# Performance work log

Hardware: AMD Instinct MI355X
Metric: run time of the kernel (lower is better)

## Reference

```python
import jax, jax.numpy as jnp
import numpy as np

B, R, C, E = 4, 32, 512, 512
H = 8
D = E // H  # 64
EPS = 1e-6


def setup_inputs() -> dict:
    key = jax.random.key(0)
    ks = jax.random.split(key, 9)
    s = 1.0 / np.sqrt(E)  # keep activations in a sane range
    return {
        "x": jax.random.normal(ks[0], (B, R, C, E), jnp.float32),
        "Wq": jax.random.normal(ks[1], (E, E), jnp.float32) * s,
        "bq": jax.random.normal(ks[2], (E,), jnp.float32) * 0.01,
        "Wk": jax.random.normal(ks[3], (E, E), jnp.float32) * s,
        "bk": jax.random.normal(ks[4], (E,), jnp.float32) * 0.01,
        "Wv": jax.random.normal(ks[5], (E, E), jnp.float32) * s,
        "bv": jax.random.normal(ks[6], (E,), jnp.float32) * 0.01,
        "Wo": jax.random.normal(ks[7], (E, E), jnp.float32) * s,
        "bo": jax.random.normal(ks[8], (E,), jnp.float32) * 0.01,
    }


def reference(x, Wq, bq, Wk, bk, Wv, bv, Wo, bo):
    b, r, c, e = x.shape
    # projections (torch Linear: y = x @ W.T + b), split heads -> [b,r,c,H,D]
    q = (x @ Wq.T + bq).reshape(b, r, c, H, D)
    k = (x @ Wk.T + bk).reshape(b, r, c, H, D)
    v = (x @ Wv.T + bv).reshape(b, r, c, H, D)
    # ELU+1 feature map (Performer/linear attention)
    q = jax.nn.elu(q) + 1.0
    k = jax.nn.elu(k) + 1.0
    # K^T V accumulation over the column axis: [b,r,H,D,D]
    ktv = jnp.einsum('brchd,brche->brhde', k, v)
    # normalizer: q . sum_c(k)  -> [b,r,c,H]
    ksum = k.sum(axis=2)  # [b,r,H,D]
    z = 1.0 / (jnp.einsum('brchd,brhd->brch', q, ksum) + EPS)
    # O(N) attention output: [b,r,c,H,D]
    out_h = jnp.einsum('brchd,brhde->brche', q, ktv) * z[..., None]
    out = out_h.reshape(b, r, c, e)
    return out @ Wo.T + bo
```

## Files before the change

### kernel.cpp

```cpp
#include <hip/hip_runtime.h>

typedef unsigned short u16;
typedef short short8 __attribute__((ext_vector_type(8)));
typedef float f32x4 __attribute__((ext_vector_type(4)));

__device__ __forceinline__ u16 f2b(float f) {
  unsigned u = __float_as_uint(f);
  u = u + 0x7FFFu + ((u >> 16) & 1u);
  return (u16)(u >> 16);
}
__device__ __forceinline__ float b2f(u16 b) {
  return __uint_as_float(((unsigned)b) << 16);
}

#define ASYNC_LD16(g, l)                                                                   \
  __builtin_amdgcn_global_load_lds((const __attribute__((address_space(1))) void*)(g),     \
                                   (__attribute__((address_space(3))) void*)(l), 16, 0, 0)

#define BAR()                                  \
  do {                                         \
    asm volatile("" ::: "memory");             \
    __builtin_amdgcn_s_barrier();              \
    asm volatile("" ::: "memory");             \
  } while (0)

__global__ void convert_x(const float* __restrict__ x, u16* __restrict__ xb) {
  size_t i = ((size_t)blockIdx.x * 256 + threadIdx.x) * 4;
  float4 f = *(const float4*)(x + i);
  ushort4 o;
  o.x = f2b(f.x); o.y = f2b(f.y); o.z = f2b(f.z); o.w = f2b(f.w);
  *(ushort4*)(xb + i) = o;
}

__global__ void convert_w(const float* __restrict__ Wq, const float* __restrict__ Wk,
                          const float* __restrict__ Wv, const float* __restrict__ Wo,
                          u16* __restrict__ Wqkv, u16* __restrict__ Wob) {
  int idx = (blockIdx.x * 256 + threadIdx.x) * 4;
  int row = idx >> 9;
  int col = idx & 511;
  const float* src = (row < 512)    ? Wq + (size_t)row * 512
                     : (row < 1024) ? Wk + (size_t)(row - 512) * 512
                     : (row < 1536) ? Wv + (size_t)(row - 1024) * 512
                                    : Wo + (size_t)(row - 1536) * 512;
  u16* dst = (row < 1536) ? Wqkv + (size_t)row * 512 : Wob + (size_t)(row - 1536) * 512;
  float4 f = *(const float4*)(src + col);
  ushort4 o;
  o.x = f2b(f.x); o.y = f2b(f.y); o.z = f2b(f.z); o.w = f2b(f.w);
  *(ushort4*)(dst + col) = o;
}


#define STAGE_A(buf, kt)                                                 \
  do {                                                                   \
    ASYNC_LD16(Asrc0 + (kt) * 32, S + (buf) * 16384 + tid * 8);          \
    ASYNC_LD16(Asrc1 + (kt) * 32, S + (buf) * 16384 + 4096 + tid * 8);   \
  } while (0)
#define STAGE_B(buf, kt)                                                 \
  do {                                                                   \
    ASYNC_LD16(Bsrc0 + (kt) * 32, S + (buf) * 16384 + 8192 + tid * 8);   \
    ASYNC_LD16(Bsrc1 + (kt) * 32, S + (buf) * 16384 + 12288 + tid * 8);  \
  } while (0)

#define GEMM_MAIN_LOOP()                                                                     \
  STAGE_A(0, 0); STAGE_B(0, 0);                                                              \
  STAGE_A(1, 1); STAGE_B(1, 1);                                                              \
  STAGE_A(2, 2); STAGE_B(2, 2);                                                              \
  asm volatile("s_waitcnt vmcnt(8)" ::: "memory");               \
  BAR();                                                                                     \
  for (int t = 0; t < 16; ++t) {                                                             \
    const u16* Ab = S + (t & 3) * 16384;                                                     \
    const int nb = (t + 3) & 3;                                                              \
    short8 bf[4], af[4];                                                                     \
                     \
    if (t < 13) STAGE_A(nb, t + 3);                                                          \
    _Pragma("unroll") for (int j = 0; j < 4; ++j) bf[j] = *(const short8*)&Ab[rbB + j * 512];\
    _Pragma("unroll") for (int m = 0; m < 4; ++m) af[m] = *(const short8*)&Ab[rbA + m * 512];\
    BAR();                                                                                   \
    __builtin_amdgcn_s_setprio(1);                                                           \
    _Pragma("unroll") for (int m = 0; m < 4; ++m)                                            \
      _Pragma("unroll") for (int j = 0; j < 4; ++j)                                          \
        acc[m][j] = __builtin_amdgcn_mfma_f32_16x16x32_bf16(af[m], bf[j], acc[m][j], 0, 0, 0);\
    __builtin_amdgcn_s_setprio(0);                                                           \
                               \
    if (t < 13) STAGE_B(nb, t + 3);                                                          \
    _Pragma("unroll") for (int m = 0; m < 4; ++m)                                            \
        af[m] = *(const short8*)&Ab[rbA + (m + 4) * 512];                                    \
    BAR();                                                                                   \
    __builtin_amdgcn_s_setprio(1);                                                           \
    _Pragma("unroll") for (int m = 0; m < 4; ++m)                                            \
      _Pragma("unroll") for (int j = 0; j < 4; ++j)                                          \
        acc[m + 4][j] =                                                                      \
            __builtin_amdgcn_mfma_f32_16x16x32_bf16(af[m], bf[j], acc[m + 4][j], 0, 0, 0);   \
    __builtin_amdgcn_s_setprio(0);                                                           \
         \
    if (t < 13)      asm volatile("s_waitcnt vmcnt(8)" ::: "memory");                        \
    else if (t == 13) asm volatile("s_waitcnt vmcnt(4)" ::: "memory");                       \
    else             asm volatile("s_waitcnt vmcnt(0)" ::: "memory");                        \
    BAR();                                                                                   \
  }

__global__ __launch_bounds__(512, 2) void gemm_qkv(
    const u16* __restrict__ xb, const u16* __restrict__ Wqkv,
    const float* __restrict__ bq, const float* __restrict__ bk,
    const float* __restrict__ bv, u16* __restrict__ Qb,
    u16* __restrict__ Ktg, u16* __restrict__ Vtg) {
  __shared__ u16 S[65536];
  const int tid = threadIdx.x;
  const int bid = blockIdx.x;
  const int wg = (bid & 7) * 192 + (bid >> 3);
  const int mtile = wg / 6;
  const int ntile = wg - mtile * 6;
  const int blockM = mtile << 8;
  const int blockN = ntile << 8;

  const int lane = tid & 63;
  const int w = tid >> 6;
  const int wm = (w >> 2) << 7;
  const int wn = (w & 3) << 6;
  const int lr = lane & 15;
  const int qd = lane >> 4;

  const int srow = tid >> 2;
  const int sg = (tid & 3) ^ ((tid >> 3) & 3);
  const u16* Asrc0 = xb + (size_t)(blockM + srow) * 512 + sg * 8;
  const u16* Asrc1 = Asrc0 + 128 * 512;
  const u16* Bsrc0 = Wqkv + (size_t)(blockN + srow) * 512 + sg * 8;
  const u16* Bsrc1 = Bsrc0 + 128 * 512;

  const int gsw = (qd ^ ((lr >> 1) & 3)) * 8;
  const int rbA = (wm + lr) * 32 + gsw;
  const int rbB = 8192 + (wn + lr) * 32 + gsw;

  f32x4 acc[8][4];
#pragma unroll
  for (int m = 0; m < 8; ++m)
#pragma unroll
    for (int j = 0; j < 4; ++j) acc[m][j] = {0.f, 0.f, 0.f, 0.f};

  GEMM_MAIN_LOOP();

  const int which = blockN >> 9;
  const int cb = blockN & 511;
  if (which == 0) {
#pragma unroll
    for (int j = 0; j < 4; ++j) {
      int col = cb + wn + j * 16 + lr;
      float bsv = bq[col];
#pragma unroll
      for (int m = 0; m < 8; ++m) {
        int row = blockM + wm + m * 16 + qd * 4;
#pragma unroll
        for (int r = 0; r < 4; ++r) {
          float v = acc[m][j][r] + bsv;
          v = (v > 0.f) ? v + 1.f : __expf(v);
          Qb[(size_t)(row + r) * 512 + col] = f2b(v);
        }
      }
    }
  } else {
    u16* dstT = (which == 1) ? Ktg : Vtg;
    const float* bias = (which == 1) ? bk : bv;
    const int br = blockM >> 9;
    const int t0 = (blockM & 511) + wm;
#pragma unroll
    for (int j = 0; j < 4; ++j) {
      int col = cb + wn + j * 16 + lr;
      float bsv = bias[col];
      size_t rowbase = (size_t)br * 262144 + (size_t)col * 512;
#pragma unroll
      for (int m = 0; m < 8; ++m) {
        int c0 = t0 + m * 16 + qd * 4;
        float v0 = acc[m][j][0] + bsv, v1 = acc[m][j][1] + bsv;
        float v2 = acc[m][j][2] + bsv, v3 = acc[m][j][3] + bsv;
        if (which == 1) {
          v0 = (v0 > 0.f) ? v0 + 1.f : __expf(v0);
          v1 = (v1 > 0.f) ? v1 + 1.f : __expf(v1);
          v2 = (v2 > 0.f) ? v2 + 1.f : __expf(v2);
          v3 = (v3 > 0.f) ? v3 + 1.f : __expf(v3);
        }
        ushort4 p;
        p.x = f2b(v0); p.y = f2b(v1); p.z = f2b(v2); p.w = f2b(v3);
        *(ushort4*)&dstT[rowbase + c0] = p;
      }
    }
  }
}

__global__ void attn(const u16* __restrict__ Qb, const u16* __restrict__ Ktg,
                     const u16* __restrict__ Vtg, u16* __restrict__ Hb) {
  __shared__ u16 KtS[64 * 32];
  __shared__ u16 VtS[64 * 32];
  __shared__ u16 QS[2 * 128 * 32];
  __shared__ u16 ktvT[2 * 64 * 32];
  __shared__ float part[256];
  __shared__ float ksumf[64];
  __shared__ float zs[128];

  const int tid = threadIdx.x;
  const int br = blockIdx.x >> 3;
  const int h = blockIdx.x & 7;
  const int h64 = h * 64;
  const size_t tok0 = (size_t)br * 512;
  const size_t tbase = (size_t)br * 262144 + (size_t)h64 * 512;

  const int lane = tid & 63;
  const int w = tid >> 6;
  const int lr = lane & 15;
  const int qd = lane >> 4;

  const int sc_chan = tid >> 2, sc_seg = tid & 3;

  f32x4 acc[4];
#pragma unroll
  for (int j = 0; j < 4; ++j) acc[j] = {0.f, 0.f, 0.f, 0.f};
  float ks = 0.f;

  for (int ct = 0; ct < 16; ++ct) {
    __syncthreads();
    {
      size_t g = tbase + (size_t)sc_chan * 512 + ct * 32 + sc_seg * 8;
      ASYNC_LD16(Ktg + g, KtS + tid * 8);
      ASYNC_LD16(Vtg + g, VtS + tid * 8);
    }
    __syncthreads();
    short8 a = *(const short8*)&KtS[(w * 16 + lr) * 32 + qd * 8];
#pragma unroll
    for (int j = 0; j < 4; ++j) {
      short8 b = *(const short8*)&VtS[(j * 16 + lr) * 32 + qd * 8];
      acc[j] = __builtin_amdgcn_mfma_f32_16x16x32_bf16(a, b, acc[j], 0, 0, 0);
    }
    ushort4 k0 = *(const ushort4*)&KtS[sc_chan * 32 + sc_seg * 8];
    ushort4 k1 = *(const ushort4*)&KtS[sc_chan * 32 + sc_seg * 8 + 4];
    ks += b2f(k0.x) + b2f(k0.y) + b2f(k0.z) + b2f(k0.w)
        + b2f(k1.x) + b2f(k1.y) + b2f(k1.z) + b2f(k1.w);
  }
  part[tid] = ks;
  {
    int kc = w >> 1;
    int dp = (w & 1) * 16 + qd * 4;
#pragma unroll
    for (int j = 0; j < 4; ++j) {
      int e = j * 16 + lr;
      ushort4 p;
      p.x = f2b(acc[j][0]); p.y = f2b(acc[j][1]);
      p.z = f2b(acc[j][2]); p.w = f2b(acc[j][3]);
      *(ushort4*)&ktvT[kc * 2048 + e * 32 + dp] = p;
    }
  }
  __syncthreads();
  if (tid < 64)
    ksumf[tid] = part[tid * 4] + part[tid * 4 + 1] + part[tid * 4 + 2] + part[tid * 4 + 3];
  __syncthreads();

  short8 bfr[4][2];
#pragma unroll
  for (int j = 0; j < 4; ++j)
#pragma unroll
    for (int kc = 0; kc < 2; ++kc)
      bfr[j][kc] = *(const short8*)&ktvT[kc * 2048 + (j * 16 + lr) * 32 + qd * 8];

  for (int ct = 0; ct < 4; ++ct) {
    __syncthreads();
#pragma unroll
    for (int kc = 0; kc < 2; ++kc)
#pragma unroll
      for (int half = 0; half < 2; ++half)
        ASYNC_LD16(Qb + (tok0 + ct * 128 + half * 64 + sc_chan) * 512 + h64 + kc * 32 + sc_seg * 8,
                   QS + kc * 4096 + half * 2048 + tid * 8);
    __syncthreads();
    if (tid < 128) {
      float s = 0.f;
#pragma unroll 8
      for (int i = 0; i < 32; ++i) {
        int ix = (i + tid) & 31;
        s += b2f(QS[tid * 32 + ix]) * ksumf[ix];
        s += b2f(QS[4096 + tid * 32 + ix]) * ksumf[32 + ix];
      }
      zs[tid] = 1.f / (s + 1e-6f);
    }
    __syncthreads();
#pragma unroll
    for (int s = 0; s < 2; ++s) {
      int mrow = (w * 2 + s) * 16 + lr;
      short8 a0 = *(const short8*)&QS[mrow * 32 + qd * 8];
      short8 a1 = *(const short8*)&QS[4096 + mrow * 32 + qd * 8];
      f32x4 o[4];
#pragma unroll
      for (int j = 0; j < 4; ++j) {
        o[j] = {0.f, 0.f, 0.f, 0.f};
        o[j] = __builtin_amdgcn_mfma_f32_16x16x32_bf16(a0, bfr[j][0], o[j], 0, 0, 0);
        o[j] = __builtin_amdgcn_mfma_f32_16x16x32_bf16(a1, bfr[j][1], o[j], 0, 0, 0);
      }
      int tl = (w * 2 + s) * 16 + qd * 4;
      float z0 = zs[tl], z1 = zs[tl + 1], z2 = zs[tl + 2], z3 = zs[tl + 3];
      size_t gb = (tok0 + ct * 128 + tl) * 512 + h64;
#pragma unroll
      for (int j = 0; j < 4; ++j) {
        int e = j * 16 + lr;
        Hb[gb + e] = f2b(o[j][0] * z0);
        Hb[gb + 512 + e] = f2b(o[j][1] * z1);
        Hb[gb + 1024 + e] = f2b(o[j][2] * z2);
        Hb[gb + 1536 + e] = f2b(o[j][3] * z3);
      }
    }
  }
}

__global__ __launch_bounds__(512, 2) void gemm_out(
    const u16* __restrict__ Hb, const u16* __restrict__ Wob,
    const float* __restrict__ bo, float* __restrict__ out) {
  __shared__ u16 S[65536];
  const int tid = threadIdx.x;
  const int bid = blockIdx.x;
  const int wg = (bid & 7) * 64 + (bid >> 3);
  const int mtile = wg >> 1;
  const int ntile = wg & 1;
  const int blockM = mtile << 8;
  const int blockN = ntile << 8;

  const int lane = tid & 63;
  const int w = tid >> 6;
  const int wm = (w >> 2) << 7;
  const int wn = (w & 3) << 6;
  const int lr = lane & 15;
  const int qd = lane >> 4;

  const int srow = tid >> 2;
  const int sg = (tid & 3) ^ ((tid >> 3) & 3);
  const u16* Asrc0 = Hb + (size_t)(blockM + srow) * 512 + sg * 8;
  const u16* Asrc1 = Asrc0 + 128 * 512;
  const u16* Bsrc0 = Wob + (size_t)(blockN + srow) * 512 + sg * 8;
  const u16* Bsrc1 = Bsrc0 + 128 * 512;

  const int gsw = (qd ^ ((lr >> 1) & 3)) * 8;
  const int rbA = (wm + lr) * 32 + gsw;
  const int rbB = 8192 + (wn + lr) * 32 + gsw;

  f32x4 acc[8][4];
#pragma unroll
  for (int m = 0; m < 8; ++m)
#pragma unroll
    for (int j = 0; j < 4; ++j) acc[m][j] = {0.f, 0.f, 0.f, 0.f};

  GEMM_MAIN_LOOP();

#pragma unroll
  for (int j = 0; j < 4; ++j) {
    int col = blockN + wn + j * 16 + lr;
    float bsv = bo[col];
#pragma unroll
    for (int m = 0; m < 8; ++m) {
      int row = blockM + wm + m * 16 + qd * 4;
#pragma unroll
      for (int r = 0; r < 4; ++r)
        out[(size_t)(row + r) * 512 + col] = acc[m][j][r] + bsv;
    }
  }
}

extern "C" void kernel_launch(void* const* d_in, const int* in_sizes, int n_in,
                              void* d_out, int out_size, void* d_ws, size_t ws_size,
                              hipStream_t stream) {
  const float* x  = (const float*)d_in[0];
  const float* Wq = (const float*)d_in[1];
  const float* bq = (const float*)d_in[2];
  const float* Wk = (const float*)d_in[3];
  const float* bk = (const float*)d_in[4];
  const float* Wv = (const float*)d_in[5];
  const float* bv = (const float*)d_in[6];
  const float* Wo = (const float*)d_in[7];
  const float* bo = (const float*)d_in[8];
  float* out = (float*)d_out;

  char* ws = (char*)d_ws;
  u16* xb   = (u16*)(ws);
  u16* Wqkv = (u16*)(ws + 0x04000000ull);
  u16* Wob  = (u16*)(ws + 0x04200000ull);
  u16* Qb   = (u16*)(ws + 0x04400000ull);
  u16* Ktg  = (u16*)(ws + 0x08400000ull);
  u16* Vtg  = (u16*)(ws + 0x0C400000ull);
  u16* Hb   = xb;

  hipLaunchKernelGGL(convert_x, dim3(32768), dim3(256), 0, stream, x, xb);
  hipLaunchKernelGGL(convert_w, dim3(1024), dim3(256), 0, stream, Wq, Wk, Wv, Wo, Wqkv, Wob);
  hipLaunchKernelGGL(gemm_qkv, dim3(1536), dim3(512), 0, stream, xb, Wqkv, bq, bk, bv, Qb, Ktg, Vtg);
  hipLaunchKernelGGL(attn, dim3(1024), dim3(256), 0, stream, Qb, Ktg, Vtg, Hb);
  hipLaunchKernelGGL(gemm_out, dim3(512), dim3(512), 0, stream, Hb, Wob, bo, out);
}
```

Baseline: 487.0 us.

## Restructure GEMM main loop to K=64 double-buffered stages with quadrant MFMA clusters

Replaces the 4-stage K=32 async-load pipeline with a 2-buffer K=64 scheme, where each buffer holds A and B tiles with a new 8-way XOR swizzle. Each K-step is split into four MFMA clusters over output quadrants. The next tile's global-to-LDS loads are interleaved between clusters, with fewer loop iterations and a different barrier cadence. The goal is to cut barrier and loop overhead per MFMA and to overlap loads with compute better. In exchange the prefetch distance is shallower, there are more barriers per step, and the register pressure from the two-slice fragments is higher.

```diff
diff --git a/kernel.cpp b/kernel.cpp
--- a/kernel.cpp
+++ b/kernel.cpp
@@ -50,53 +50,86 @@
 }
 
 
-#define STAGE_A(buf, kt)                                                 \
-  do {                                                                   \
-    ASYNC_LD16(Asrc0 + (kt) * 32, S + (buf) * 16384 + tid * 8);          \
-    ASYNC_LD16(Asrc1 + (kt) * 32, S + (buf) * 16384 + 4096 + tid * 8);   \
+#define LDSV(off) (*(const short8*)&S[(off)])
+
+#define STG(gp, scol, dst)                              \
+  do {                                                  \
+    ASYNC_LD16((gp) + (scol), S + (dst));               \
+    ASYNC_LD16((gp) + (scol) + 4096, S + (dst) + 512);  \
   } while (0)
-#define STAGE_B(buf, kt)                                                 \
-  do {                                                                   \
-    ASYNC_LD16(Bsrc0 + (kt) * 32, S + (buf) * 16384 + 8192 + tid * 8);   \
-    ASYNC_LD16(Bsrc1 + (kt) * 32, S + (buf) * 16384 + 12288 + tid * 8);  \
+
+#define MFMA_CL(MB, JB)                                                                     \
+  do {                                                                                      \
+    __builtin_amdgcn_s_setprio(1);                                                          \
+    _Pragma("unroll") for (int m_ = 0; m_ < 4; ++m_)                                        \
+      _Pragma("unroll") for (int j_ = 0; j_ < 2; ++j_) {                                    \
+        acc[(MB) + m_][(JB) + j_] = __builtin_amdgcn_mfma_f32_16x16x32_bf16(                \
+            aq[m_][0], bf[(JB) + j_][0], acc[(MB) + m_][(JB) + j_], 0, 0, 0);               \
+        acc[(MB) + m_][(JB) + j_] = __builtin_amdgcn_mfma_f32_16x16x32_bf16(                \
+            aq[m_][1], bf[(JB) + j_][1], acc[(MB) + m_][(JB) + j_], 0, 0, 0);               \
+      }                                                                                     \
+    __builtin_amdgcn_s_setprio(0);                                                          \
   } while (0)
 
-#define GEMM_MAIN_LOOP()                                                                     \
-  STAGE_A(0, 0); STAGE_B(0, 0);                                                              \
-  STAGE_A(1, 1); STAGE_B(1, 1);                                                              \
-  STAGE_A(2, 2); STAGE_B(2, 2);                                                              \
-  asm volatile("s_waitcnt vmcnt(8)" ::: "memory");               \
+#define KSTEP(BUF, SG1, SG2, SG3, SG4, BND)                                                  \
+  do {                                                                                       \
+    short8 aq[4][2], bf[4][2];                                                               \
+                                                \
+    _Pragma("unroll") for (int m_ = 0; m_ < 4; ++m_) {                                       \
+      aq[m_][0] = LDSV((BUF) + rA0 + m_ * 1024);                                             \
+      aq[m_][1] = LDSV((BUF) + rA1 + m_ * 1024);                                             \
+    }                                                                                        \
+    _Pragma("unroll") for (int j_ = 0; j_ < 2; ++j_) {                                       \
+      bf[j_][0] = LDSV((BUF) + rB0 + j_ * 1024);                                             \
+      bf[j_][1] = LDSV((BUF) + rB1 + j_ * 1024);                                             \
+    }                                                                                        \
+    SG1;                                                                                     \
+    BAR(); MFMA_CL(0, 0); BAR();                                                             \
+                                                                    \
+    _Pragma("unroll") for (int j_ = 0; j_ < 2; ++j_) {                                       \
+      bf[2 + j_][0] = LDSV((BUF) + rB0 + (2 + j_) * 1024);                                   \
+      bf[2 + j_][1] = LDSV((BUF) + rB1 + (2 + j_) * 1024);                                   \
+    }                                                                                        \
+    SG2; BAR(); MFMA_CL(0, 2); BAR();                                                        \
+                                  \
+    _Pragma("unroll") for (int m_ = 0; m_ < 4; ++m_) {                                       \
+      aq[m_][0] = LDSV((BUF) + rA0 + (4 + m_) * 1024);                                       \
+      aq[m_][1] = LDSV((BUF) + rA1 + (4 + m_) * 1024);                                       \
+    }                                                                                        \
+    SG3; BAR(); MFMA_CL(4, 2); BAR();                                                        \
+                                                                           \
+    SG4; BAR(); MFMA_CL(4, 0); BND; BAR();                                                   \
+  } while (0)
+
+#define GEMM8_LOOP()                                                                         \
+  STG(gB0, 0, dB0); STG(gB1, 0, dB1);                                                        \
+  STG(gA0, 0, dA0); STG(gA1, 0, dA1);                                                        \
+  STG(gB0, 64, 32768 + dB0); STG(gB1, 64, 32768 + dB1);                                      \
+  asm volatile("s_waitcnt vmcnt(4)" ::: "memory");                                           \
   BAR();                                                                                     \
-  for (int t = 0; t < 16; ++t) {                                                             \
-    const u16* Ab = S + (t & 3) * 16384;                                                     \
-    const int nb = (t + 3) & 3;                                                              \
-    short8 bf[4], af[4];                                                                     \
-                     \
-    if (t < 13) STAGE_A(nb, t + 3);                                                          \
-    _Pragma("unroll") for (int j = 0; j < 4; ++j) bf[j] = *(const short8*)&Ab[rbB + j * 512];\
-    _Pragma("unroll") for (int m = 0; m < 4; ++m) af[m] = *(const short8*)&Ab[rbA + m * 512];\
-    BAR();                                                                                   \
-    __builtin_amdgcn_s_setprio(1);                                                           \
-    _Pragma("unroll") for (int m = 0; m < 4; ++m)                                            \
-      _Pragma("unroll") for (int j = 0; j < 4; ++j)                                          \
-        acc[m][j] = __builtin_amdgcn_mfma_f32_16x16x32_bf16(af[m], bf[j], acc[m][j], 0, 0, 0);\
-    __builtin_amdgcn_s_setprio(0);                                                           \
-                               \
-    if (t < 13) STAGE_B(nb, t + 3);                                                          \
-    _Pragma("unroll") for (int m = 0; m < 4; ++m)                                            \
-        af[m] = *(const short8*)&Ab[rbA + (m + 4) * 512];                                    \
-    BAR();                                                                                   \
-    __builtin_amdgcn_s_setprio(1);                                                           \
-    _Pragma("unroll") for (int m = 0; m < 4; ++m)                                            \
-      _Pragma("unroll") for (int j = 0; j < 4; ++j)                                          \
-        acc[m + 4][j] =                                                                      \
-            __builtin_amdgcn_mfma_f32_16x16x32_bf16(af[m], bf[j], acc[m + 4][j], 0, 0, 0);   \
-    __builtin_amdgcn_s_setprio(0);                                                           \
-         \
-    if (t < 13)      asm volatile("s_waitcnt vmcnt(8)" ::: "memory");                        \
-    else if (t == 13) asm volatile("s_waitcnt vmcnt(4)" ::: "memory");                       \
-    else             asm volatile("s_waitcnt vmcnt(0)" ::: "memory");                        \
-    BAR();                                                                                   \
+  _Pragma("unroll") for (int i = 0; i < 4; ++i) {                                            \
+    const int s1c = (2 * i + 1) * 64, s2c = (2 * i + 2) * 64, s3c = (2 * i + 3) * 64;        \
+    if (i < 3) {                                                                             \
+      KSTEP(0,                                                                               \
+            STG(gA0, s1c, 32768 + dA0),                                                      \
+            STG(gA1, s1c, 32768 + dA1),                                                      \
+            STG(gB0, s2c, dB0),                                                              \
+            STG(gB1, s2c, dB1),                                                              \
+            asm volatile("s_waitcnt vmcnt(4)" ::: "memory"));                                \
+      KSTEP(32768,                                                                           \
+            STG(gA0, s2c, dA0),                                                              \
+            STG(gA1, s2c, dA1),                                                              \
+            STG(gB0, s3c, 32768 + dB0),                                                      \
+            STG(gB1, s3c, 32768 + dB1),                                                      \
+            asm volatile("s_waitcnt vmcnt(4)" ::: "memory"));                                \
+    } else {                                                                                 \
+      KSTEP(0,                                                                               \
+            STG(gA0, s1c, 32768 + dA0),                                                      \
+            STG(gA1, s1c, 32768 + dA1),                                                      \
+            (void)0, (void)0,                                                                \
+            asm volatile("s_waitcnt vmcnt(0)" ::: "memory"));                                \
+      KSTEP(32768, (void)0, (void)0, (void)0, (void)0, (void)0);                             \
+    }                                                                                        \
   }
 
 __global__ __launch_bounds__(512, 2) void gemm_qkv(
@@ -119,17 +152,24 @@
   const int wn = (w & 3) << 6;
   const int lr = lane & 15;
   const int qd = lane >> 4;
-
-  const int srow = tid >> 2;
-  const int sg = (tid & 3) ^ ((tid >> 3) & 3);
-  const u16* Asrc0 = xb + (size_t)(blockM + srow) * 512 + sg * 8;
-  const u16* Asrc1 = Asrc0 + 128 * 512;
-  const u16* Bsrc0 = Wqkv + (size_t)(blockN + srow) * 512 + sg * 8;
-  const u16* Bsrc1 = Bsrc0 + 128 * 512;
-
-  const int gsw = (qd ^ ((lr >> 1) & 3)) * 8;
-  const int rbA = (wm + lr) * 32 + gsw;
-  const int rbB = 8192 + (wn + lr) * 32 + gsw;
+  const int r7 = lr & 7;
+  const int l8 = lane >> 3;
+  const int l7 = lane & 7;
+
+  const int gsw8 = (l7 ^ l8) * 8;
+  const u16* gA0 = xb + (size_t)(blockM + w * 16 + l8) * 512 + gsw8;
+  const u16* gA1 = gA0 + 128 * 512;
+  const u16* gB0 = Wqkv + (size_t)(blockN + w * 16 + l8) * 512 + gsw8;
+  const u16* gB1 = gB0 + 128 * 512;
+  const int dA0 = (w * 16 + l8) * 64 + l7 * 8;
+  const int dA1 = dA0 + 8192;
+  const int dB0 = dA0 + 16384;
+  const int dB1 = dA0 + 24576;
+
+  const int rA0 = (wm + lr) * 64 + ((qd) ^ r7) * 8;
+  const int rA1 = (wm + lr) * 64 + ((qd + 4) ^ r7) * 8;
+  const int rB0 = 16384 + (wn + lr) * 64 + ((qd) ^ r7) * 8;
+  const int rB1 = 16384 + (wn + lr) * 64 + ((qd + 4) ^ r7) * 8;
 
   f32x4 acc[8][4];
 #pragma unroll
@@ -137,7 +177,7 @@
 #pragma unroll
     for (int j = 0; j < 4; ++j) acc[m][j] = {0.f, 0.f, 0.f, 0.f};
 
-  GEMM_MAIN_LOOP();
+  GEMM8_LOOP();
 
   const int which = blockN >> 9;
   const int cb = blockN & 511;
@@ -324,17 +364,24 @@
   const int wn = (w & 3) << 6;
   const int lr = lane & 15;
   const int qd = lane >> 4;
-
-  const int srow = tid >> 2;
-  const int sg = (tid & 3) ^ ((tid >> 3) & 3);
-  const u16* Asrc0 = Hb + (size_t)(blockM + srow) * 512 + sg * 8;
-  const u16* Asrc1 = Asrc0 + 128 * 512;
-  const u16* Bsrc0 = Wob + (size_t)(blockN + srow) * 512 + sg * 8;
-  const u16* Bsrc1 = Bsrc0 + 128 * 512;
-
-  const int gsw = (qd ^ ((lr >> 1) & 3)) * 8;
-  const int rbA = (wm + lr) * 32 + gsw;
-  const int rbB = 8192 + (wn + lr) * 32 + gsw;
+  const int r7 = lr & 7;
+  const int l8 = lane >> 3;
+  const int l7 = lane & 7;
+
+  const int gsw8 = (l7 ^ l8) * 8;
+  const u16* gA0 = Hb + (size_t)(blockM + w * 16 + l8) * 512 + gsw8;
+  const u16* gA1 = gA0 + 128 * 512;
+  const u16* gB0 = Wob + (size_t)(blockN + w * 16 + l8) * 512 + gsw8;
+  const u16* gB1 = gB0 + 128 * 512;
+  const int dA0 = (w * 16 + l8) * 64 + l7 * 8;
+  const int dA1 = dA0 + 8192;
+  const int dB0 = dA0 + 16384;
+  const int dB1 = dA0 + 24576;
+
+  const int rA0 = (wm + lr) * 64 + ((qd) ^ r7) * 8;
+  const int rA1 = (wm + lr) * 64 + ((qd + 4) ^ r7) * 8;
+  const int rB0 = 16384 + (wn + lr) * 64 + ((qd) ^ r7) * 8;
+  const int rB1 = 16384 + (wn + lr) * 64 + ((qd + 4) ^ r7) * 8;
 
   f32x4 acc[8][4];
 #pragma unroll
@@ -342,7 +389,7 @@
 #pragma unroll
     for (int j = 0; j < 4; ++j) acc[m][j] = {0.f, 0.f, 0.f, 0.f};
 
-  GEMM_MAIN_LOOP();
+  GEMM8_LOOP();
 
 #pragma unroll
   for (int j = 0; j < 4; ++j) {
```

New measurement: 465.6 us. 1.05x faster.
